# Optimization experiments

Hardware: AMD Instinct MI355X
Metric: run time of the kernel (lower is better)

Reference implementation:

```python
import jax, jax.numpy as jnp
import numpy as np

N, E, H, L = 20000, 640000, 128, 3
IN_NODE, IN_EDGE = 128, 128


def _ln(x):
    m = jnp.mean(x, -1, keepdims=True)
    v = jnp.mean((x - m) ** 2, -1, keepdims=True)
    return (x - m) / jnp.sqrt(v + 1e-5)


def _multi_aggr(msg, dst, n):
    # PyG MultiAggregation(['mean','std','max','min']) -> concat on feature dim
    cnt = jax.ops.segment_sum(jnp.ones((msg.shape[0],), msg.dtype), dst, n)
    denom = jnp.maximum(cnt, 1.0)[:, None]
    mean = jax.ops.segment_sum(msg, dst, n) / denom
    mean2 = jax.ops.segment_sum(msg * msg, dst, n) / denom
    std = jnp.sqrt(jax.nn.relu(mean2 - mean * mean) + 1e-5)  # PyG StdAggregation
    has = (cnt > 0)[:, None]
    mx = jnp.where(has, jax.ops.segment_max(msg, dst, n), 0.0)
    mn = jnp.where(has, jax.ops.segment_min(msg, dst, n), 0.0)
    return jnp.concatenate([mean, std, mx, mn], axis=-1)  # [n, 4H]


def _pna(h, src, dst, ea, W1, b1, W2, b2, W3, b3, W4, b4, Wd, bd, n):
    # flow='source_to_target': j = src = edge_index[0], i = dst = edge_index[1]
    x1 = jax.nn.silu(h @ W1 + b1)  # lin1 -> x_j
    z = jax.nn.silu(h @ W2 + b2)   # lin2 -> z_i
    msg = z[dst] * x1[src] * ea    # message = z_i * x_j * edge_attr
    ret_node = _multi_aggr(msg, dst, n) @ Wd + bd
    ret_edge = jax.nn.silu(h @ W3 + b3)[src] * jax.nn.silu(h @ W4 + b4)[dst] * ea
    return ret_node, ret_edge


def _gnn(x, edge_index, edge_attr, Wn, bn, We, be, W1, b1, W2, b2, W3, b3, W4, b4,
         Wd, bd, Wnd1, bnd1, Wnd2, bnd2, Wed1, bed1, Wed2, bed2):
    n = x.shape[0]
    h = Wn.shape[1]
    src, dst = edge_index[0], edge_index[1]
    inv = jnp.concatenate([jnp.ones((h // 2,), x.dtype), -jnp.ones(((h + 1) // 2,), x.dtype)])
    hidden = x @ Wn + bn
    in_ea = edge_attr
    ea = edge_attr @ We + be
    for i in range(W1.shape[0]):
        hn = _ln(hidden)
        rn1, re1 = _pna(hn, src, dst, ea, W1[i], b1[i], W2[i], b2[i], W3[i], b3[i], W4[i], b4[i], Wd[i], bd[i], n)
        rn2, re2 = _pna(hn, dst, src, inv * ea, W1[i], b1[i], W2[i], b2[i], W3[i], b3[i], W4[i], b4[i], Wd[i], bd[i], n)
        hidden = hidden + rn1 + rn2
        ea = ea + re1 + inv * re2
    node_pred = x + 0.01 * (jax.nn.silu(_ln(hidden) @ Wnd1 + bnd1) @ Wnd2 + bnd2)
    edge_pred = in_ea + 0.01 * (jax.nn.silu(_ln(ea) @ Wed1 + bed1) @ Wed2 + bed2)
    return node_pred, edge_pred


def setup_inputs() -> dict:
    key = jax.random.key(0)
    ks = jax.random.split(key, 20)
    g = lambda k, s, sc=0.05: jax.random.normal(k, s, jnp.float32) * sc
    return {
        "x": g(ks[0], (N, IN_NODE), 1.0),
        "edge_attr": g(ks[1], (E, IN_EDGE), 1.0),
        "Wn": g(ks[2], (IN_NODE, H)), "bn": jnp.zeros((H,), jnp.float32),
        "We": g(ks[3], (IN_EDGE, H)), "be": jnp.zeros((H,), jnp.float32),
        "W1": g(ks[4], (L, H, H)), "b1": jnp.zeros((L, H), jnp.float32),
        "W2": g(ks[5], (L, H, H)), "b2": jnp.zeros((L, H), jnp.float32),
        "W3": g(ks[6], (L, H, H)), "b3": jnp.zeros((L, H), jnp.float32),
        "W4": g(ks[7], (L, H, H)), "b4": jnp.zeros((L, H), jnp.float32),
        "Wd": g(ks[8], (L, 4 * H, H)), "bd": jnp.zeros((L, H), jnp.float32),
        "Wnd1": g(ks[9], (H, H)), "bnd1": jnp.zeros((H,), jnp.float32),
        "Wnd2": g(ks[10], (H, IN_NODE)), "bnd2": jnp.zeros((IN_NODE,), jnp.float32),
        "Wed1": g(ks[11], (H, H)), "bed1": jnp.zeros((H,), jnp.float32),
        "Wed2": g(ks[12], (H, IN_EDGE)), "bed2": jnp.zeros((IN_EDGE,), jnp.float32),
        "edge_index": jax.random.randint(ks[13], (2, E), 0, N),
    }


def reference(x, edge_attr, Wn, bn, We, be, W1, b1, W2, b2, W3, b3, W4, b4, Wd, bd,
              Wnd1, bnd1, Wnd2, bnd2, Wed1, bed1, Wed2, bed2, edge_index):
    return _gnn(x, edge_index, edge_attr, Wn, bn, We, be, W1, b1, W2, b2, W3, b3,
                W4, b4, Wd, bd, Wnd1, bnd1, Wnd2, bnd2, Wed1, bed1, Wed2, bed2)
```

## Files before the change

kernel.cpp:

```cpp
#include <hip/hip_runtime.h>
#include <cstdint>
#include <cstddef>

typedef __attribute__((ext_vector_type(8))) short short8x;
typedef __attribute__((ext_vector_type(4))) float f32x4;

static constexpr int NN = 20000;
static constexpr int EE = 640000;
static constexpr int NT_E = EE / 128;
static constexpr int NPAIR = NT_E / 2;

#define DEVI __device__ __forceinline__

DEVI float b2f(uint16_t u){ union{uint32_t i; float f;} x; x.i = (uint32_t)u<<16; return x.f; }
DEVI uint16_t f2b(float f){ union{float f; uint32_t i;} x; x.f=f; uint32_t i=x.i;
  return (uint16_t)((i + 0x7FFFu + ((i>>16)&1u))>>16); }
DEVI float silu_f(float v){ return v / (1.f + __expf(-v)); }

DEVI uint4 pack8(float4 a, float4 b){
  union{uint16_t u[8]; uint4 q;} pk;
  pk.u[0]=f2b(a.x); pk.u[1]=f2b(a.y); pk.u[2]=f2b(a.z); pk.u[3]=f2b(a.w);
  pk.u[4]=f2b(b.x); pk.u[5]=f2b(b.y); pk.u[6]=f2b(b.z); pk.u[7]=f2b(b.w);
  return pk.q;
}
DEVI uint2 pack4(float4 a){
  union{uint16_t u[4]; uint2 q;} pk;
  pk.u[0]=f2b(a.x); pk.u[1]=f2b(a.y); pk.u[2]=f2b(a.z); pk.u[3]=f2b(a.w);
  return pk.q;
}
DEVI float4 unpk4(uint2 v){
  return (float4){ b2f((uint16_t)(v.x & 0xFFFFu)), b2f((uint16_t)(v.x >> 16)),
                   b2f((uint16_t)(v.y & 0xFFFFu)), b2f((uint16_t)(v.y >> 16)) };
}

DEVI void ln8(float4& a, float4& b){
  float s = a.x+a.y+a.z+a.w + b.x+b.y+b.z+b.w;
  float q = a.x*a.x+a.y*a.y+a.z*a.z+a.w*a.w + b.x*b.x+b.y*b.y+b.z*b.z+b.w*b.w;
#pragma unroll
  for (int d=1; d<16; d<<=1){ s += __shfl_xor(s,d); q += __shfl_xor(q,d); }
  float m = s * 0.0078125f;
  float rstd = rsqrtf(fmaxf(q*0.0078125f - m*m, 0.f) + 1e-5f);
  a.x=(a.x-m)*rstd; a.y=(a.y-m)*rstd; a.z=(a.z-m)*rstd; a.w=(a.w-m)*rstd;
  b.x=(b.x-m)*rstd; b.y=(b.y-m)*rstd; b.z=(b.z-m)*rstd; b.w=(b.w-m)*rstd;
}

template<int AF32, int LNA, int EPI, int SILU>
__global__ __launch_bounds__(256) void gemm_node(
    const void* Ap, const uint16_t* __restrict__ Wt,
    const float* __restrict__ bias, float bias_scale,
    int M, int K,
    uint16_t* outb, float* outf,
    const float* __restrict__ resid, float resid_scale)
{
  __shared__ uint16_t Als[128*136];
  __shared__ uint16_t Wls[128*136];
  const int t = threadIdx.x;
  const int row0 = blockIdx.x * 128;
  const int w = t >> 6, l = t & 63;
  const int lr = l & 15, lk = (l>>4)*8;

  f32x4 acc[2][8];
#pragma unroll
  for (int a=0;a<2;a++)
#pragma unroll
    for(int b=0;b<8;b++) acc[a][b] = (f32x4){0.f,0.f,0.f,0.f};

  for (int kc = 0; kc < K; kc += 128){
#pragma unroll
    for (int i=0;i<8;i++){
      int c = t + i*256;
      int r = c >> 4, k8 = (c & 15)*8;
      int gr = row0 + r;
      if (AF32){
        float4 a = {0.f,0.f,0.f,0.f}, b = {0.f,0.f,0.f,0.f};
        if (gr < M){
          const float* Af = (const float*)Ap + (size_t)gr*K + kc + k8;
          a = *(const float4*)Af; b = *(const float4*)(Af + 4);
        }
        if (LNA) ln8(a, b);
        *(uint4*)(&Als[r*136 + k8]) = pack8(a, b);
      } else {
        uint4 v = {0u,0u,0u,0u};
        if (gr < M) v = *(const uint4*)((const uint16_t*)Ap + (size_t)gr*K + kc + k8);
        *(uint4*)(&Als[r*136 + k8]) = v;
      }
    }
#pragma unroll
    for (int i=0;i<8;i++){
      int c = t + i*256;
      int r = c >> 4, k8 = (c & 15)*8;
      *(uint4*)(&Wls[r*136 + k8]) = *(const uint4*)(Wt + (size_t)r*K + kc + k8);
    }
    __syncthreads();
#pragma unroll
    for (int kt=0; kt<4; ++kt){
      int kb = kt*32 + lk;
      short8x bfr[8];
#pragma unroll
      for (int c16=0;c16<8;c16++) bfr[c16] = *(const short8x*)(&Wls[(c16*16+lr)*136 + kb]);
#pragma unroll
      for (int r16=0;r16<2;r16++){
        short8x afr = *(const short8x*)(&Als[(w*32 + r16*16 + lr)*136 + kb]);
#pragma unroll
        for (int c16=0;c16<8;c16++)
          acc[r16][c16] = __builtin_amdgcn_mfma_f32_16x16x32_bf16(bfr[c16], afr, acc[r16][c16], 0,0,0);
      }
    }
    __syncthreads();
  }

  float4 bbv[8];
#pragma unroll
  for (int c16=0;c16<8;c16++){
    float4 b4 = *(const float4*)(bias + c16*16 + (l>>4)*4);
    bbv[c16] = (float4){b4.x*bias_scale, b4.y*bias_scale, b4.z*bias_scale, b4.w*bias_scale};
  }
#pragma unroll
  for (int r16=0;r16<2;r16++){
    int row = row0 + w*32 + r16*16 + lr;
    if (row >= M) continue;
#pragma unroll
    for (int c16=0;c16<8;c16++){
      int colb = c16*16 + (l>>4)*4;
      float4 v = (float4){acc[r16][c16][0]+bbv[c16].x, acc[r16][c16][1]+bbv[c16].y,
                          acc[r16][c16][2]+bbv[c16].z, acc[r16][c16][3]+bbv[c16].w};
      if (SILU){ v.x=silu_f(v.x); v.y=silu_f(v.y); v.z=silu_f(v.z); v.w=silu_f(v.w); }
      size_t o = (size_t)row*128 + colb;
      if (EPI==0)      *(uint2*)(outb + o) = pack4(v);
      else if (EPI==1) *(float4*)(outf + o) = v;
      else if (EPI==2){ float4 old = *(const float4*)(outf + o);
        *(float4*)(outf + o) = (float4){old.x+v.x, old.y+v.y, old.z+v.z, old.w+v.w}; }
      else { float4 r = *(const float4*)(resid + o);
        *(float4*)(outf + o) = (float4){r.x+resid_scale*v.x, r.y+resid_scale*v.y,
                                        r.z+resid_scale*v.z, r.w+resid_scale*v.w}; }
    }
  }
}

__global__ __launch_bounds__(256) void proj4(
    const float* __restrict__ hidden, const uint16_t* __restrict__ Wt4,
    const float* __restrict__ b0p, const float* __restrict__ b1p,
    const float* __restrict__ b2p, const float* __restrict__ b3p,
    uint16_t* o0, uint16_t* o1, uint16_t* o2, uint16_t* o3, int M)
{
  __shared__ uint16_t Als[128*136];
  __shared__ uint16_t Wls[2][128*136];
  const int t = threadIdx.x;
  const int row0 = blockIdx.x * 128;
  const int w = t >> 6, l = t & 63;
  const int lr = l & 15, lk = (l>>4)*8;

#pragma unroll
  for (int i=0;i<8;i++){
    int c = t + i*256;
    int r = c >> 4, k8 = (c & 15)*8;
    int gr = row0 + r;
    float4 a = {0.f,0.f,0.f,0.f}, b = {0.f,0.f,0.f,0.f};
    if (gr < M){
      const float* Af = hidden + (size_t)gr*128 + k8;
      a = *(const float4*)Af; b = *(const float4*)(Af + 4);
    }
    ln8(a, b);
    *(uint4*)(&Als[r*136 + k8]) = pack8(a, b);
  }
#pragma unroll
  for (int i=0;i<8;i++){
    int c = t + i*256;
    int r = c >> 4, k8 = (c & 15)*8;
    *(uint4*)(&Wls[0][r*136 + k8]) = *(const uint4*)(Wt4 + (size_t)r*128 + k8);
  }
  __syncthreads();

#pragma unroll
  for (int p=0; p<4; ++p){
    if (p < 3){
#pragma unroll
      for (int i=0;i<8;i++){
        int c = t + i*256;
        int r = c >> 4, k8 = (c & 15)*8;
        *(uint4*)(&Wls[(p+1)&1][r*136 + k8]) =
          *(const uint4*)(Wt4 + (size_t)(p+1)*16384 + (size_t)r*128 + k8);
      }
    }
    f32x4 acc[2][8];
#pragma unroll
    for (int a=0;a<2;a++)
#pragma unroll
      for(int b=0;b<8;b++) acc[a][b] = (f32x4){0.f,0.f,0.f,0.f};
#pragma unroll
    for (int kt=0; kt<4; ++kt){
      int kb = kt*32 + lk;
      short8x bfr[8];
#pragma unroll
      for (int c16=0;c16<8;c16++) bfr[c16] = *(const short8x*)(&Wls[p&1][(c16*16+lr)*136 + kb]);
#pragma unroll
      for (int r16=0;r16<2;r16++){
        short8x afr = *(const short8x*)(&Als[(w*32 + r16*16 + lr)*136 + kb]);
#pragma unroll
        for (int c16=0;c16<8;c16++)
          acc[r16][c16] = __builtin_amdgcn_mfma_f32_16x16x32_bf16(bfr[c16], afr, acc[r16][c16], 0,0,0);
      }
    }
    const float* bp = (p==0)?b0p:(p==1)?b1p:(p==2)?b2p:b3p;
    uint16_t* op = (p==0)?o0:(p==1)?o1:(p==2)?o2:o3;
#pragma unroll
    for (int r16=0;r16<2;r16++){
      int row = row0 + w*32 + r16*16 + lr;
      if (row >= M) continue;
#pragma unroll
      for (int c16=0;c16<8;c16++){
        int colb = c16*16 + (l>>4)*4;
        float4 b4 = *(const float4*)(bp + colb);
        float4 v = (float4){silu_f(acc[r16][c16][0]+b4.x), silu_f(acc[r16][c16][1]+b4.y),
                            silu_f(acc[r16][c16][2]+b4.z), silu_f(acc[r16][c16][3]+b4.w)};
        *(uint2*)(op + (size_t)row*128 + colb) = pack4(v);
      }
    }
    __syncthreads();
  }
}

__global__ __launch_bounds__(256, 2) void enc_edge(
    const float* __restrict__ A, const uint16_t* __restrict__ Wt,
    const float* __restrict__ bias, float* __restrict__ outf)
{
  __shared__ uint16_t Als[128*136];
  __shared__ uint16_t Wls[128*136];
  const int t = threadIdx.x;
  const int w = t >> 6, l = t & 63;
  const int lr = l & 15, lk = (l>>4)*8;

#pragma unroll
  for (int i=0;i<8;i++){
    int c = t + i*256;
    int r = c >> 4, k8 = (c & 15)*8;
    *(uint4*)(&Wls[r*136 + k8]) = *(const uint4*)(Wt + (size_t)r*128 + k8);
  }
  float4 bbv[8];
#pragma unroll
  for (int c16=0;c16<8;c16++) bbv[c16] = *(const float4*)(bias + c16*16 + (l>>4)*4);

  int tile = blockIdx.x;
  float4 va[16];
#pragma unroll
  for (int i=0;i<8;i++){
    int c = t + i*256; int r = c>>4, k8 = (c&15)*8;
    const float* Af = A + ((size_t)tile*128 + r)*128 + k8;
    va[2*i] = *(const float4*)Af; va[2*i+1] = *(const float4*)(Af + 4);
  }
  while (tile < NT_E){
#pragma unroll
    for (int i=0;i<8;i++){
      int c = t + i*256; int r = c>>4, k8 = (c&15)*8;
      *(uint4*)(&Als[r*136 + k8]) = pack8(va[2*i], va[2*i+1]);
    }
    int next = tile + (int)gridDim.x;
    if (next < NT_E){
#pragma unroll
      for (int i=0;i<8;i++){
        int c = t + i*256; int r = c>>4, k8 = (c&15)*8;
        const float* Af = A + ((size_t)next*128 + r)*128 + k8;
        va[2*i] = *(const float4*)Af; va[2*i+1] = *(const float4*)(Af + 4);
      }
    }
    __syncthreads();
    f32x4 acc[2][8];
#pragma unroll
    for (int a=0;a<2;a++)
#pragma unroll
      for(int b=0;b<8;b++) acc[a][b] = (f32x4){0.f,0.f,0.f,0.f};
#pragma unroll
    for (int kt=0; kt<4; ++kt){
      int kb = kt*32 + lk;
      short8x bfr[8];
#pragma unroll
      for (int c16=0;c16<8;c16++) bfr[c16] = *(const short8x*)(&Wls[(c16*16+lr)*136 + kb]);
#pragma unroll
      for (int r16=0;r16<2;r16++){
        short8x afr = *(const short8x*)(&Als[(w*32 + r16*16 + lr)*136 + kb]);
#pragma unroll
        for (int c16=0;c16<8;c16++)
          acc[r16][c16] = __builtin_amdgcn_mfma_f32_16x16x32_bf16(bfr[c16], afr, acc[r16][c16], 0,0,0);
      }
    }
#pragma unroll
    for (int r16=0;r16<2;r16++){
      size_t row = (size_t)tile*128 + w*32 + r16*16 + lr;
#pragma unroll
      for (int c16=0;c16<8;c16++){
        int colb = c16*16 + (l>>4)*4;
        *(float4*)(outf + row*128 + colb) =
          (float4){acc[r16][c16][0]+bbv[c16].x, acc[r16][c16][1]+bbv[c16].y,
                   acc[r16][c16][2]+bbv[c16].z, acc[r16][c16][3]+bbv[c16].w};
      }
    }
    __syncthreads();
    tile = next;
  }
}

__global__ __launch_bounds__(512) void dec_edge(
    const float* __restrict__ ea, const float* __restrict__ eatt,
    const uint16_t* __restrict__ W1t, const uint16_t* __restrict__ W2t,
    const float* __restrict__ b1, const float* __restrict__ b2,
    float* __restrict__ outf)
{
  __shared__ uint16_t Als[2][128*136];
  __shared__ uint16_t W1ls[128*136];
  __shared__ uint16_t W2ls[128*136];
  const int t = threadIdx.x;
  const int half = t >> 8, th = t & 255;
  const int w = t >> 6, l = t & 63;
  const int lr = l & 15, lk = (l>>4)*8;
  const int tsel = w >> 2, wloc = w & 3;

#pragma unroll
  for (int i=0;i<4;i++){
    int c = t + i*512;
    int r = c >> 4, k8 = (c & 15)*8;
    *(uint4*)(&W1ls[r*136 + k8]) = *(const uint4*)(W1t + (size_t)r*128 + k8);
    *(uint4*)(&W2ls[r*136 + k8]) = *(const uint4*)(W2t + (size_t)r*128 + k8);
  }
  float bb1[8];
  float4 bb2v[8];
#pragma unroll
  for (int c16=0;c16<8;c16++){
    bb1[c16] = b1[c16*16+lr];
    bb2v[c16] = *(const float4*)(b2 + c16*16 + (l>>4)*4);
  }

  int pr = blockIdx.x;
  float4 va[16];
  float4 vet[16];
#pragma unroll
  for (int i=0;i<8;i++){
    int c = th + i*256; int r = c>>4, k8 = (c&15)*8;
    const float* Af = ea + ((size_t)pr*256 + half*128 + r)*128 + k8;
    va[2*i] = *(const float4*)Af; va[2*i+1] = *(const float4*)(Af + 4);
  }
#pragma unroll
  for (int r16=0;r16<2;r16++)
#pragma unroll
    for (int c16=0;c16<8;c16++){
      size_t row = (size_t)pr*256 + tsel*128 + wloc*32 + r16*16 + lr;
      vet[r16*8+c16] = *(const float4*)(eatt + row*128 + c16*16 + (l>>4)*4);
    }

  while (pr < NPAIR){
#pragma unroll
    for (int i=0;i<8;i++){
      int c = th + i*256; int r = c>>4, k8 = (c&15)*8;
      float4 a = va[2*i], b = va[2*i+1];
      ln8(a, b);
      *(uint4*)(&Als[half][r*136 + k8]) = pack8(a, b);
    }
    int nx = pr + (int)gridDim.x;
    if (nx < NPAIR){
#pragma unroll
      for (int i=0;i<8;i++){
        int c = th + i*256; int r = c>>4, k8 = (c&15)*8;
        const float* Af = ea + ((size_t)nx*256 + half*128 + r)*128 + k8;
        va[2*i] = *(const float4*)Af; va[2*i+1] = *(const float4*)(Af + 4);
      }
    }
    __syncthreads();

    f32x4 acc[2][8];
#pragma unroll
    for (int a=0;a<2;a++)
#pragma unroll
      for(int b=0;b<8;b++) acc[a][b] = (f32x4){0.f,0.f,0.f,0.f};
#pragma unroll
    for (int kt=0; kt<4; ++kt){
      int kb = kt*32 + lk;
      short8x bfr[8];
#pragma unroll
      for (int c16=0;c16<8;c16++) bfr[c16] = *(const short8x*)(&W1ls[(c16*16+lr)*136 + kb]);
#pragma unroll
      for (int r16=0;r16<2;r16++){
        short8x afr = *(const short8x*)(&Als[tsel][(wloc*32 + r16*16 + lr)*136 + kb]);
#pragma unroll
        for (int c16=0;c16<8;c16++)
          acc[r16][c16] = __builtin_amdgcn_mfma_f32_16x16x32_bf16(afr, bfr[c16], acc[r16][c16], 0,0,0);
      }
    }
#pragma unroll
    for (int r16=0;r16<2;r16++)
#pragma unroll
      for (int c16=0;c16<8;c16++)
#pragma unroll
        for (int j=0;j<4;j++){
          int rloc = wloc*32 + r16*16 + (l>>4)*4 + j;
          Als[tsel][rloc*136 + c16*16 + lr] = f2b(silu_f(acc[r16][c16][j] + bb1[c16]));
        }
    f32x4 acc2[2][8];
#pragma unroll
    for (int a=0;a<2;a++)
#pragma unroll
      for(int b=0;b<8;b++) acc2[a][b] = (f32x4){0.f,0.f,0.f,0.f};
#pragma unroll
    for (int kt=0; kt<4; ++kt){
      int kb = kt*32 + lk;
      short8x bfr[8];
#pragma unroll
      for (int c16=0;c16<8;c16++) bfr[c16] = *(const short8x*)(&W2ls[(c16*16+lr)*136 + kb]);
#pragma unroll
      for (int r16=0;r16<2;r16++){
        short8x afr = *(const short8x*)(&Als[tsel][(wloc*32 + r16*16 + lr)*136 + kb]);
#pragma unroll
        for (int c16=0;c16<8;c16++)
          acc2[r16][c16] = __builtin_amdgcn_mfma_f32_16x16x32_bf16(bfr[c16], afr, acc2[r16][c16], 0,0,0);
      }
    }
#pragma unroll
    for (int r16=0;r16<2;r16++){
      size_t row = (size_t)pr*256 + tsel*128 + wloc*32 + r16*16 + lr;
#pragma unroll
      for (int c16=0;c16<8;c16++){
        int colb = c16*16 + (l>>4)*4;
        float4 e = vet[r16*8+c16];
        *(float4*)(outf + row*128 + colb) =
          (float4){e.x + 0.01f*(acc2[r16][c16][0]+bb2v[c16].x),
                   e.y + 0.01f*(acc2[r16][c16][1]+bb2v[c16].y),
                   e.z + 0.01f*(acc2[r16][c16][2]+bb2v[c16].z),
                   e.w + 0.01f*(acc2[r16][c16][3]+bb2v[c16].w)};
      }
    }
    if (nx < NPAIR){
#pragma unroll
      for (int r16=0;r16<2;r16++)
#pragma unroll
        for (int c16=0;c16<8;c16++){
          size_t row = (size_t)nx*256 + tsel*128 + wloc*32 + r16*16 + lr;
          vet[r16*8+c16] = *(const float4*)(eatt + row*128 + c16*16 + (l>>4)*4);
        }
    }
    __syncthreads();
    pr = nx;
  }
}

template<int INV, int EUPD, int ACCUM>
__global__ __launch_bounds__(128) void agg_kernel(
    const float* __restrict__ ea, float* ea_out,
    const uint16_t* __restrict__ x1, const uint16_t* __restrict__ z,
    const uint16_t* __restrict__ h3, const uint16_t* __restrict__ h4,
    const int* __restrict__ eids, const int* __restrict__ ptr,
    const int* __restrict__ other, uint16_t* stats)
{
  __shared__ int se[128];
  __shared__ int so[128];
  __shared__ float red[4][4][128];
  const int i = blockIdx.x, t = threadIdx.x;
  const int g = t >> 5, q = t & 31;
  const int f0 = q*4;
  float4 zi = unpk4(*(const uint2*)(z + (size_t)i*128 + f0));
  float4 h3i = {0,0,0,0}, h4i = {0,0,0,0};
  if (EUPD){
    h3i = unpk4(*(const uint2*)(h3 + (size_t)i*128 + f0));
    h4i = unpk4(*(const uint2*)(h4 + (size_t)i*128 + f0));
  }
  const int beg = ptr[i], end = ptr[i+1];
  float4 s={0,0,0,0}, s2={0,0,0,0};
  float4 mx={-3.4e38f,-3.4e38f,-3.4e38f,-3.4e38f}, mn={3.4e38f,3.4e38f,3.4e38f,3.4e38f};
  for (int jb = beg; jb < end; jb += 128){
    int cn = min(128, end - jb);
    if (t < cn){ int e = eids[jb+t]; se[t] = e; so[t] = other[e]; }
    __syncthreads();
#pragma unroll 2
    for (int jj = g; jj < cn; jj += 4){
      int e = se[jj], o = so[jj];
      float4 xo = unpk4(*(const uint2*)(x1 + (size_t)o*128 + f0));
      float4 ev = *(const float4*)(ea + (size_t)e*128 + f0);
      float4 m = (float4){zi.x*xo.x*ev.x, zi.y*xo.y*ev.y, zi.z*xo.z*ev.z, zi.w*xo.w*ev.w};
      if (INV){ if (q >= 16){ m.x=-m.x; m.y=-m.y; m.z=-m.z; m.w=-m.w; } }
      s.x+=m.x; s.y+=m.y; s.z+=m.z; s.w+=m.w;
      s2.x+=m.x*m.x; s2.y+=m.y*m.y; s2.z+=m.z*m.z; s2.w+=m.w*m.w;
      mx.x=fmaxf(mx.x,m.x); mx.y=fmaxf(mx.y,m.y); mx.z=fmaxf(mx.z,m.z); mx.w=fmaxf(mx.w,m.w);
      mn.x=fminf(mn.x,m.x); mn.y=fminf(mn.y,m.y); mn.z=fminf(mn.z,m.z); mn.w=fminf(mn.w,m.w);
      if (EUPD){
        float4 h3o = unpk4(*(const uint2*)(h3 + (size_t)o*128 + f0));
        float4 h4o = unpk4(*(const uint2*)(h4 + (size_t)o*128 + f0));
        *(float4*)(ea_out + (size_t)e*128 + f0) =
          (float4){ev.x*(1.f + h3o.x*h4i.x + h3i.x*h4o.x),
                   ev.y*(1.f + h3o.y*h4i.y + h3i.y*h4o.y),
                   ev.z*(1.f + h3o.z*h4i.z + h3i.z*h4o.z),
                   ev.w*(1.f + h3o.w*h4i.w + h3i.w*h4o.w)};
      }
    }
    __syncthreads();
  }
  *(float4*)(&red[g][0][f0]) = s;
  *(float4*)(&red[g][1][f0]) = s2;
  *(float4*)(&red[g][2][f0]) = mx;
  *(float4*)(&red[g][3][f0]) = mn;
  __syncthreads();
  float fs = red[0][0][t]+red[1][0][t]+red[2][0][t]+red[3][0][t];
  float fq = red[0][1][t]+red[1][1][t]+red[2][1][t]+red[3][1][t];
  float fmx = fmaxf(fmaxf(red[0][2][t],red[1][2][t]), fmaxf(red[2][2][t],red[3][2][t]));
  float fmn = fminf(fminf(red[0][3][t],red[1][3][t]), fminf(red[2][3][t],red[3][3][t]));
  int cnt = end - beg;
  float dn = cnt > 0 ? 1.f/(float)cnt : 1.f;
  float mean = fs*dn, m2 = fq*dn;
  float sd = sqrtf(fmaxf(m2 - mean*mean, 0.f) + 1e-5f);
  if (cnt == 0){ fmx = 0.f; fmn = 0.f; }
  size_t o0 = (size_t)i*512 + t;
  if (ACCUM){
    stats[o0    ] = f2b(b2f(stats[o0    ]) + mean);
    stats[o0+128] = f2b(b2f(stats[o0+128]) + sd);
    stats[o0+256] = f2b(b2f(stats[o0+256]) + fmx);
    stats[o0+384] = f2b(b2f(stats[o0+384]) + fmn);
  } else {
    stats[o0]=f2b(mean); stats[o0+128]=f2b(sd); stats[o0+256]=f2b(fmx); stats[o0+384]=f2b(fmn);
  }
}

__global__ void count_deg(const int* __restrict__ ei, int* cnt_src, int* cnt_dst){
  int e = blockIdx.x*256 + threadIdx.x;
  if (e < EE){
    atomicAdd(&cnt_src[ei[e]], 1);
    atomicAdd(&cnt_dst[ei[EE+e]], 1);
  }
}

__global__ __launch_bounds__(1024) void scan20k(const int* __restrict__ cnt, int* ptr){
  __shared__ int buf[1024];
  constexpr int C = 20;
  int t = threadIdx.x;
  int base = t*C;
  int loc[C];
  int sum = 0;
#pragma unroll
  for (int j=0;j<C;j++){
    int idx = base+j;
    int v = (idx < NN) ? cnt[idx] : 0;
    loc[j] = sum; sum += v;
  }
  buf[t] = sum;
  __syncthreads();
  for (int sft=1; sft<1024; sft<<=1){
    int add = (t>=sft) ? buf[t-sft] : 0;
    __syncthreads();
    buf[t] += add;
    __syncthreads();
  }
  int excl = buf[t] - sum;
#pragma unroll
  for (int j=0;j<C;j++){
    int idx = base+j;
    if (idx < NN) ptr[idx] = excl + loc[j];
  }
  if (t == 1023) ptr[NN] = buf[1023];
}

__global__ void init_cursor(const int* p1, int* c1, const int* p2, int* c2, int n){
  int i = blockIdx.x*256 + threadIdx.x;
  if (i < n){ c1[i] = p1[i]; c2[i] = p2[i]; }
}

__global__ void scatter_edges(const int* __restrict__ ei, int* cur_src, int* cur_dst,
                              int* eid_src, int* eid_dst){
  int e = blockIdx.x*256 + threadIdx.x;
  if (e < EE){
    int s = ei[e], d = ei[EE+e];
    eid_src[atomicAdd(&cur_src[s],1)] = e;
    eid_dst[atomicAdd(&cur_dst[d],1)] = e;
  }
}

__global__ void transpose_w(const float* __restrict__ W, uint16_t* __restrict__ Wt,
                            int K, int total){
  int idx = blockIdx.x*256 + threadIdx.x;
  if (idx < total){
    int per = K*128;
    int m = idx / per, r = idx - m*per;
    int k = r >> 7, c = r & 127;
    Wt[(size_t)m*per + (size_t)c*K + k] = f2b(W[idx]);
  }
}

extern "C" void kernel_launch(void* const* d_in, const int* in_sizes, int n_in,
                              void* d_out, int out_size, void* d_ws, size_t ws_size,
                              hipStream_t stream)
{
  const float* x    = (const float*)d_in[0];
  const float* eatt = (const float*)d_in[1];
  const float* Wn   = (const float*)d_in[2];
  const float* bn   = (const float*)d_in[3];
  const float* We   = (const float*)d_in[4];
  const float* be   = (const float*)d_in[5];
  const float* W1   = (const float*)d_in[6];
  const float* b1   = (const float*)d_in[7];
  const float* W2   = (const float*)d_in[8];
  const float* b2   = (const float*)d_in[9];
  const float* W3   = (const float*)d_in[10];
  const float* b3   = (const float*)d_in[11];
  const float* W4   = (const float*)d_in[12];
  const float* b4   = (const float*)d_in[13];
  const float* Wd   = (const float*)d_in[14];
  const float* bd   = (const float*)d_in[15];
  const float* Wnd1 = (const float*)d_in[16];
  const float* bnd1 = (const float*)d_in[17];
  const float* Wnd2 = (const float*)d_in[18];
  const float* bnd2 = (const float*)d_in[19];
  const float* Wed1 = (const float*)d_in[20];
  const float* bed1 = (const float*)d_in[21];
  const float* Wed2 = (const float*)d_in[22];
  const float* bed2 = (const float*)d_in[23];
  const int* ei     = (const int*)d_in[24];

  float* out_node = (float*)d_out;
  float* out_edge = out_node + (size_t)NN*128;
  float* ea = out_edge;

  char* p = (char*)d_ws;
  auto alloc = [&](size_t bytes)->char*{
    char* r = p; p += (bytes + 255) & ~(size_t)255; return r; };

  float*    hidden = (float*)   alloc((size_t)NN*128*4);
  uint16_t* x1b    = (uint16_t*)alloc((size_t)NN*128*2);
  uint16_t* zb     = (uint16_t*)alloc((size_t)NN*128*2);
  uint16_t* h3b    = (uint16_t*)alloc((size_t)NN*128*2);
  uint16_t* h4b    = (uint16_t*)alloc((size_t)NN*128*2);
  uint16_t* stats  = (uint16_t*)alloc((size_t)NN*512*2);
  int* cnt_src = (int*)alloc((size_t)NN*4);
  int* cnt_dst = (int*)alloc((size_t)NN*4);
  int* ptr_src = (int*)alloc((size_t)(NN+1)*4);
  int* ptr_dst = (int*)alloc((size_t)(NN+1)*4);
  int* cur_src = (int*)alloc((size_t)NN*4);
  int* cur_dst = (int*)alloc((size_t)NN*4);
  int* eid_src = (int*)alloc((size_t)EE*4);
  int* eid_dst = (int*)alloc((size_t)EE*4);
  uint16_t* WT = (uint16_t*)alloc((size_t)491520*2);

  uint16_t* wnT   = WT;
  uint16_t* weT   = WT + 16384;
  uint16_t* w1T   = WT + 32768;
  uint16_t* w2T   = WT + 81920;
  uint16_t* w3T   = WT + 131072;
  uint16_t* w4T   = WT + 180224;
  uint16_t* wdT   = WT + 229376;
  uint16_t* wnd1T = WT + 425984;
  uint16_t* wnd2T = WT + 442368;
  uint16_t* wed1T = WT + 458752;
  uint16_t* wed2T = WT + 475136;

  uint16_t* wp4 = (uint16_t*)alloc((size_t)3*4*16384*2);

  hipMemsetAsync(cnt_src, 0, (size_t)NN*4, stream);
  hipMemsetAsync(cnt_dst, 0, (size_t)NN*4, stream);
  count_deg<<<(EE+255)/256, 256, 0, stream>>>(ei, cnt_src, cnt_dst);
  scan20k<<<1, 1024, 0, stream>>>(cnt_src, ptr_src);
  scan20k<<<1, 1024, 0, stream>>>(cnt_dst, ptr_dst);
  init_cursor<<<(NN+255)/256, 256, 0, stream>>>(ptr_src, cur_src, ptr_dst, cur_dst, NN);
  scatter_edges<<<(EE+255)/256, 256, 0, stream>>>(ei, cur_src, cur_dst, eid_src, eid_dst);

  transpose_w<<<64, 256, 0, stream>>>(Wn, wnT, 128, 16384);
  transpose_w<<<64, 256, 0, stream>>>(We, weT, 128, 16384);
  transpose_w<<<192, 256, 0, stream>>>(W1, w1T, 128, 49152);
  transpose_w<<<192, 256, 0, stream>>>(W2, w2T, 128, 49152);
  transpose_w<<<192, 256, 0, stream>>>(W3, w3T, 128, 49152);
  transpose_w<<<192, 256, 0, stream>>>(W4, w4T, 128, 49152);
  transpose_w<<<768, 256, 0, stream>>>(Wd, wdT, 512, 196608);
  transpose_w<<<64, 256, 0, stream>>>(Wnd1, wnd1T, 128, 16384);
  transpose_w<<<64, 256, 0, stream>>>(Wnd2, wnd2T, 128, 16384);
  transpose_w<<<64, 256, 0, stream>>>(Wed1, wed1T, 128, 16384);
  transpose_w<<<64, 256, 0, stream>>>(Wed2, wed2T, 128, 16384);
  for (int lyr = 0; lyr < 3; ++lyr){
    hipMemcpyAsync(wp4 + (size_t)lyr*65536 +     0, w1T + lyr*16384, 32768, hipMemcpyDeviceToDevice, stream);
    hipMemcpyAsync(wp4 + (size_t)lyr*65536 + 16384, w2T + lyr*16384, 32768, hipMemcpyDeviceToDevice, stream);
    hipMemcpyAsync(wp4 + (size_t)lyr*65536 + 32768, w3T + lyr*16384, 32768, hipMemcpyDeviceToDevice, stream);
    hipMemcpyAsync(wp4 + (size_t)lyr*65536 + 49152, w4T + lyr*16384, 32768, hipMemcpyDeviceToDevice, stream);
  }

  const int gN = (NN+127)/128;

  gemm_node<1,0,1,0><<<gN, 256, 0, stream>>>(x, wnT, bn, 1.f, NN, 128, nullptr, hidden, nullptr, 0.f);
  enc_edge<<<512, 256, 0, stream>>>(eatt, weT, be, ea);

  for (int lyr = 0; lyr < 3; ++lyr){
    const uint16_t* wdl = wdT + lyr*65536;
    proj4<<<gN, 256, 0, stream>>>(hidden, wp4 + (size_t)lyr*65536,
                                  b1 + lyr*128, b2 + lyr*128, b3 + lyr*128, b4 + lyr*128,
                                  x1b, zb, h3b, h4b, NN);
    agg_kernel<1,0,0><<<NN, 128, 0, stream>>>(ea, nullptr, x1b, zb, nullptr, nullptr,
                                              eid_src, ptr_src, ei + EE, stats);
    agg_kernel<0,1,1><<<NN, 128, 0, stream>>>(ea, ea, x1b, zb, h3b, h4b,
                                              eid_dst, ptr_dst, ei, stats);
    gemm_node<0,0,2,0><<<gN, 256, 0, stream>>>(stats, wdl, bd + lyr*128, 2.f, NN, 512, nullptr, hidden, nullptr, 0.f);
  }

  gemm_node<1,1,0,1><<<gN, 256, 0, stream>>>(hidden, wnd1T, bnd1, 1.f, NN, 128, x1b, nullptr, nullptr, 0.f);
  gemm_node<0,0,3,0><<<gN, 256, 0, stream>>>(x1b, wnd2T, bnd2, 1.f, NN, 128, nullptr, out_node, x, 0.01f);

  dec_edge<<<256, 512, 0, stream>>>(ea, eatt, wed1T, wed2T, bed1, bed2, out_edge);
}
```

Baseline: 1.705 ms.

## Store edge features in bf16 workspace and simplify edge encoder/decoder kernels

Keeps the running edge-feature tensor in a bf16 workspace buffer when there is room, instead of fp32 in the output buffer. This halves the bytes moved by the edge-bound aggregation kernels in every layer. The edge encoder and decoder are rewritten to read MFMA fragments straight from global memory, one tile per block, with no persistent loop and no shared-memory staging. W1-W4 are now transposed straight into the packed layout, removing the device copies. The cost is extra rounding error that builds up in edge features over the three layers.

After: 1.401 ms. -17.8%, faster.

```diff
diff --git a/kernel.cpp b/kernel.cpp
--- a/kernel.cpp
+++ b/kernel.cpp
@@ -8,7 +8,6 @@
 static constexpr int NN = 20000;
 static constexpr int EE = 640000;
 static constexpr int NT_E = EE / 128;
-static constexpr int NPAIR = NT_E / 2;
 
 #define DEVI __device__ __forceinline__
 
@@ -31,6 +30,36 @@
 DEVI float4 unpk4(uint2 v){
   return (float4){ b2f((uint16_t)(v.x & 0xFFFFu)), b2f((uint16_t)(v.x >> 16)),
                    b2f((uint16_t)(v.y & 0xFFFFu)), b2f((uint16_t)(v.y >> 16)) };
+}
+DEVI short8x pk_frag(float4 a, float4 b){
+  union{uint16_t u[8]; short8x s;} pk;
+  pk.u[0]=f2b(a.x); pk.u[1]=f2b(a.y); pk.u[2]=f2b(a.z); pk.u[3]=f2b(a.w);
+  pk.u[4]=f2b(b.x); pk.u[5]=f2b(b.y); pk.u[6]=f2b(b.z); pk.u[7]=f2b(b.w);
+  return pk.s;
+}
+
+template<typename EAT>
+DEVI void load8e(const EAT* base, size_t row, int col8, float4& a, float4& b){
+  if constexpr (sizeof(EAT)==2){
+    uint4 v = *(const uint4*)((const uint16_t*)base + row*128 + col8);
+    a = (float4){b2f((uint16_t)(v.x&0xFFFFu)), b2f((uint16_t)(v.x>>16)),
+                 b2f((uint16_t)(v.y&0xFFFFu)), b2f((uint16_t)(v.y>>16))};
+    b = (float4){b2f((uint16_t)(v.z&0xFFFFu)), b2f((uint16_t)(v.z>>16)),
+                 b2f((uint16_t)(v.w&0xFFFFu)), b2f((uint16_t)(v.w>>16))};
+  } else {
+    const float* f = (const float*)base + row*128 + col8;
+    a = *(const float4*)f; b = *(const float4*)(f+4);
+  }
+}
+template<typename EAT>
+DEVI void store4e(EAT* base, size_t idx, float4 v){
+  if constexpr (sizeof(EAT)==2) *(uint2*)((uint16_t*)base + idx) = pack4(v);
+  else *(float4*)((float*)base + idx) = v;
+}
+template<typename EAT>
+DEVI float4 ld4e(const EAT* base, size_t idx){
+  if constexpr (sizeof(EAT)==2) return unpk4(*(const uint2*)((const uint16_t*)base + idx));
+  else return *(const float4*)((const float*)base + idx);
 }
 
 DEVI void ln8(float4& a, float4& b){
@@ -220,229 +249,151 @@
   }
 }
 
+template<typename EAT>
 __global__ __launch_bounds__(256, 2) void enc_edge(
     const float* __restrict__ A, const uint16_t* __restrict__ Wt,
-    const float* __restrict__ bias, float* __restrict__ outf)
+    const float* __restrict__ bias, EAT* __restrict__ out)
 {
-  __shared__ uint16_t Als[128*136];
-  __shared__ uint16_t Wls[128*136];
-  const int t = threadIdx.x;
-  const int w = t >> 6, l = t & 63;
-  const int lr = l & 15, lk = (l>>4)*8;
-
-#pragma unroll
-  for (int i=0;i<8;i++){
-    int c = t + i*256;
-    int r = c >> 4, k8 = (c & 15)*8;
-    *(uint4*)(&Wls[r*136 + k8]) = *(const uint4*)(Wt + (size_t)r*128 + k8);
-  }
-  float4 bbv[8];
-#pragma unroll
-  for (int c16=0;c16<8;c16++) bbv[c16] = *(const float4*)(bias + c16*16 + (l>>4)*4);
-
-  int tile = blockIdx.x;
-  float4 va[16];
-#pragma unroll
-  for (int i=0;i<8;i++){
-    int c = t + i*256; int r = c>>4, k8 = (c&15)*8;
-    const float* Af = A + ((size_t)tile*128 + r)*128 + k8;
-    va[2*i] = *(const float4*)Af; va[2*i+1] = *(const float4*)(Af + 4);
-  }
-  while (tile < NT_E){
-#pragma unroll
-    for (int i=0;i<8;i++){
-      int c = t + i*256; int r = c>>4, k8 = (c&15)*8;
-      *(uint4*)(&Als[r*136 + k8]) = pack8(va[2*i], va[2*i+1]);
-    }
-    int next = tile + (int)gridDim.x;
-    if (next < NT_E){
-#pragma unroll
-      for (int i=0;i<8;i++){
-        int c = t + i*256; int r = c>>4, k8 = (c&15)*8;
-        const float* Af = A + ((size_t)next*128 + r)*128 + k8;
-        va[2*i] = *(const float4*)Af; va[2*i+1] = *(const float4*)(Af + 4);
-      }
-    }
-    __syncthreads();
-    f32x4 acc[2][8];
-#pragma unroll
-    for (int a=0;a<2;a++)
-#pragma unroll
-      for(int b=0;b<8;b++) acc[a][b] = (f32x4){0.f,0.f,0.f,0.f};
-#pragma unroll
-    for (int kt=0; kt<4; ++kt){
-      int kb = kt*32 + lk;
-      short8x bfr[8];
-#pragma unroll
-      for (int c16=0;c16<8;c16++) bfr[c16] = *(const short8x*)(&Wls[(c16*16+lr)*136 + kb]);
-#pragma unroll
-      for (int r16=0;r16<2;r16++){
-        short8x afr = *(const short8x*)(&Als[(w*32 + r16*16 + lr)*136 + kb]);
-#pragma unroll
-        for (int c16=0;c16<8;c16++)
-          acc[r16][c16] = __builtin_amdgcn_mfma_f32_16x16x32_bf16(bfr[c16], afr, acc[r16][c16], 0,0,0);
-      }
-    }
-#pragma unroll
-    for (int r16=0;r16<2;r16++){
-      size_t row = (size_t)tile*128 + w*32 + r16*16 + lr;
-#pragma unroll
-      for (int c16=0;c16<8;c16++){
-        int colb = c16*16 + (l>>4)*4;
-        *(float4*)(outf + row*128 + colb) =
-          (float4){acc[r16][c16][0]+bbv[c16].x, acc[r16][c16][1]+bbv[c16].y,
-                   acc[r16][c16][2]+bbv[c16].z, acc[r16][c16][3]+bbv[c16].w};
-      }
-    }
-    __syncthreads();
-    tile = next;
-  }
-}
-
-__global__ __launch_bounds__(512) void dec_edge(
-    const float* __restrict__ ea, const float* __restrict__ eatt,
+  const int t = threadIdx.x, w = t >> 6, l = t & 63;
+  const int lr = l & 15, g = l >> 4;
+  const size_t base = (size_t)blockIdx.x*128 + w*32;
+
+  short8x fr[2][4];
+#pragma unroll
+  for (int r16=0;r16<2;r16++){
+#pragma unroll
+    for (int kt=0;kt<4;kt++){
+      const float* Af = A + (base + r16*16 + lr)*128 + kt*32 + g*8;
+      float4 a = *(const float4*)Af, b = *(const float4*)(Af + 4);
+      fr[r16][kt] = pk_frag(a, b);
+    }
+  }
+  f32x4 acc[2][8];
+#pragma unroll
+  for (int a=0;a<2;a++)
+#pragma unroll
+    for (int b=0;b<8;b++) acc[a][b] = (f32x4){0.f,0.f,0.f,0.f};
+#pragma unroll
+  for (int kt=0;kt<4;kt++){
+#pragma unroll
+    for (int c16=0;c16<8;c16++){
+      short8x bfr = *(const short8x*)(Wt + (size_t)(c16*16+lr)*128 + kt*32 + g*8);
+      acc[0][c16] = __builtin_amdgcn_mfma_f32_16x16x32_bf16(bfr, fr[0][kt], acc[0][c16], 0,0,0);
+      acc[1][c16] = __builtin_amdgcn_mfma_f32_16x16x32_bf16(bfr, fr[1][kt], acc[1][c16], 0,0,0);
+    }
+  }
+#pragma unroll
+  for (int r16=0;r16<2;r16++){
+    size_t row = base + r16*16 + lr;
+#pragma unroll
+    for (int c16=0;c16<8;c16++){
+      int colb = c16*16 + g*4;
+      float4 b4 = *(const float4*)(bias + colb);
+      store4e(out, row*128 + colb,
+        (float4){acc[r16][c16][0]+b4.x, acc[r16][c16][1]+b4.y,
+                 acc[r16][c16][2]+b4.z, acc[r16][c16][3]+b4.w});
+    }
+  }
+}
+
+template<typename EAT>
+__global__ __launch_bounds__(256, 2) void dec_edge(
+    const EAT* ea, const float* __restrict__ eatt,
     const uint16_t* __restrict__ W1t, const uint16_t* __restrict__ W2t,
     const float* __restrict__ b1, const float* __restrict__ b2,
-    float* __restrict__ outf)
+    float* outf)
 {
-  __shared__ uint16_t Als[2][128*136];
-  __shared__ uint16_t W1ls[128*136];
-  __shared__ uint16_t W2ls[128*136];
-  const int t = threadIdx.x;
-  const int half = t >> 8, th = t & 255;
-  const int w = t >> 6, l = t & 63;
-  const int lr = l & 15, lk = (l>>4)*8;
-  const int tsel = w >> 2, wloc = w & 3;
-
-#pragma unroll
-  for (int i=0;i<4;i++){
-    int c = t + i*512;
-    int r = c >> 4, k8 = (c & 15)*8;
-    *(uint4*)(&W1ls[r*136 + k8]) = *(const uint4*)(W1t + (size_t)r*128 + k8);
-    *(uint4*)(&W2ls[r*136 + k8]) = *(const uint4*)(W2t + (size_t)r*128 + k8);
-  }
-  float bb1[8];
-  float4 bb2v[8];
+  __shared__ uint16_t Pls[4][32*136];
+  const int t = threadIdx.x, w = t >> 6, l = t & 63;
+  const int lr = l & 15, g = l >> 4;
+  uint16_t* Ps = &Pls[w][0];
+  const size_t base = (size_t)blockIdx.x*128 + w*32;
+
+  short8x fr[2][4];
+#pragma unroll
+  for (int r16=0;r16<2;r16++){
+    float4 va[4][2];
+    float s=0.f, q=0.f;
+#pragma unroll
+    for (int kt=0;kt<4;kt++){
+      load8e(ea, base + r16*16 + lr, kt*32 + g*8, va[kt][0], va[kt][1]);
+      float4 a = va[kt][0], b = va[kt][1];
+      s += a.x+a.y+a.z+a.w + b.x+b.y+b.z+b.w;
+      q += a.x*a.x+a.y*a.y+a.z*a.z+a.w*a.w + b.x*b.x+b.y*b.y+b.z*b.z+b.w*b.w;
+    }
+    s += __shfl_xor(s,16); q += __shfl_xor(q,16);
+    s += __shfl_xor(s,32); q += __shfl_xor(q,32);
+    float m = s*0.0078125f;
+    float rstd = rsqrtf(fmaxf(q*0.0078125f - m*m, 0.f) + 1e-5f);
+#pragma unroll
+    for (int kt=0;kt<4;kt++){
+      float4 a = va[kt][0], b = va[kt][1];
+      a.x=(a.x-m)*rstd; a.y=(a.y-m)*rstd; a.z=(a.z-m)*rstd; a.w=(a.w-m)*rstd;
+      b.x=(b.x-m)*rstd; b.y=(b.y-m)*rstd; b.z=(b.z-m)*rstd; b.w=(b.w-m)*rstd;
+      fr[r16][kt] = pk_frag(a, b);
+    }
+  }
+  f32x4 acc[2][8];
+#pragma unroll
+  for (int a=0;a<2;a++)
+#pragma unroll
+    for (int b=0;b<8;b++) acc[a][b] = (f32x4){0.f,0.f,0.f,0.f};
+#pragma unroll
+  for (int kt=0;kt<4;kt++){
+#pragma unroll
+    for (int c16=0;c16<8;c16++){
+      short8x bfr = *(const short8x*)(W1t + (size_t)(c16*16+lr)*128 + kt*32 + g*8);
+      acc[0][c16] = __builtin_amdgcn_mfma_f32_16x16x32_bf16(fr[0][kt], bfr, acc[0][c16], 0,0,0);
+      acc[1][c16] = __builtin_amdgcn_mfma_f32_16x16x32_bf16(fr[1][kt], bfr, acc[1][c16], 0,0,0);
+    }
+  }
 #pragma unroll
   for (int c16=0;c16<8;c16++){
-    bb1[c16] = b1[c16*16+lr];
-    bb2v[c16] = *(const float4*)(b2 + c16*16 + (l>>4)*4);
-  }
-
-  int pr = blockIdx.x;
-  float4 va[16];
-  float4 vet[16];
-#pragma unroll
-  for (int i=0;i<8;i++){
-    int c = th + i*256; int r = c>>4, k8 = (c&15)*8;
-    const float* Af = ea + ((size_t)pr*256 + half*128 + r)*128 + k8;
-    va[2*i] = *(const float4*)Af; va[2*i+1] = *(const float4*)(Af + 4);
-  }
-#pragma unroll
-  for (int r16=0;r16<2;r16++)
+    float bb = b1[c16*16+lr];
+#pragma unroll
+    for (int r16=0;r16<2;r16++)
+#pragma unroll
+      for (int j=0;j<4;j++)
+        Ps[(r16*16 + g*4 + j)*136 + c16*16 + lr] = f2b(silu_f(acc[r16][c16][j] + bb));
+  }
+  f32x4 acc2[2][8];
+#pragma unroll
+  for (int a=0;a<2;a++)
+#pragma unroll
+    for (int b=0;b<8;b++) acc2[a][b] = (f32x4){0.f,0.f,0.f,0.f};
+#pragma unroll
+  for (int kt=0;kt<4;kt++){
+    short8x a0 = *(const short8x*)(Ps + (0*16 + lr)*136 + kt*32 + g*8);
+    short8x a1 = *(const short8x*)(Ps + (1*16 + lr)*136 + kt*32 + g*8);
 #pragma unroll
     for (int c16=0;c16<8;c16++){
-      size_t row = (size_t)pr*256 + tsel*128 + wloc*32 + r16*16 + lr;
-      vet[r16*8+c16] = *(const float4*)(eatt + row*128 + c16*16 + (l>>4)*4);
-    }
-
-  while (pr < NPAIR){
-#pragma unroll
-    for (int i=0;i<8;i++){
-      int c = th + i*256; int r = c>>4, k8 = (c&15)*8;
-      float4 a = va[2*i], b = va[2*i+1];
-      ln8(a, b);
-      *(uint4*)(&Als[half][r*136 + k8]) = pack8(a, b);
-    }
-    int nx = pr + (int)gridDim.x;
-    if (nx < NPAIR){
-#pragma unroll
-      for (int i=0;i<8;i++){
-        int c = th + i*256; int r = c>>4, k8 = (c&15)*8;
-        const float* Af = ea + ((size_t)nx*256 + half*128 + r)*128 + k8;
-        va[2*i] = *(const float4*)Af; va[2*i+1] = *(const float4*)(Af + 4);
-      }
-    }
-    __syncthreads();
-
-    f32x4 acc[2][8];
-#pragma unroll
-    for (int a=0;a<2;a++)
-#pragma unroll
-      for(int b=0;b<8;b++) acc[a][b] = (f32x4){0.f,0.f,0.f,0.f};
-#pragma unroll
-    for (int kt=0; kt<4; ++kt){
-      int kb = kt*32 + lk;
-      short8x bfr[8];
-#pragma unroll
-      for (int c16=0;c16<8;c16++) bfr[c16] = *(const short8x*)(&W1ls[(c16*16+lr)*136 + kb]);
-#pragma unroll
-      for (int r16=0;r16<2;r16++){
-        short8x afr = *(const short8x*)(&Als[tsel][(wloc*32 + r16*16 + lr)*136 + kb]);
-#pragma unroll
-        for (int c16=0;c16<8;c16++)
-          acc[r16][c16] = __builtin_amdgcn_mfma_f32_16x16x32_bf16(afr, bfr[c16], acc[r16][c16], 0,0,0);
-      }
-    }
-#pragma unroll
-    for (int r16=0;r16<2;r16++)
-#pragma unroll
-      for (int c16=0;c16<8;c16++)
-#pragma unroll
-        for (int j=0;j<4;j++){
-          int rloc = wloc*32 + r16*16 + (l>>4)*4 + j;
-          Als[tsel][rloc*136 + c16*16 + lr] = f2b(silu_f(acc[r16][c16][j] + bb1[c16]));
-        }
-    f32x4 acc2[2][8];
-#pragma unroll
-    for (int a=0;a<2;a++)
-#pragma unroll
-      for(int b=0;b<8;b++) acc2[a][b] = (f32x4){0.f,0.f,0.f,0.f};
-#pragma unroll
-    for (int kt=0; kt<4; ++kt){
-      int kb = kt*32 + lk;
-      short8x bfr[8];
-#pragma unroll
-      for (int c16=0;c16<8;c16++) bfr[c16] = *(const short8x*)(&W2ls[(c16*16+lr)*136 + kb]);
-#pragma unroll
-      for (int r16=0;r16<2;r16++){
-        short8x afr = *(const short8x*)(&Als[tsel][(wloc*32 + r16*16 + lr)*136 + kb]);
-#pragma unroll
-        for (int c16=0;c16<8;c16++)
-          acc2[r16][c16] = __builtin_amdgcn_mfma_f32_16x16x32_bf16(bfr[c16], afr, acc2[r16][c16], 0,0,0);
-      }
-    }
-#pragma unroll
-    for (int r16=0;r16<2;r16++){
-      size_t row = (size_t)pr*256 + tsel*128 + wloc*32 + r16*16 + lr;
-#pragma unroll
-      for (int c16=0;c16<8;c16++){
-        int colb = c16*16 + (l>>4)*4;
-        float4 e = vet[r16*8+c16];
-        *(float4*)(outf + row*128 + colb) =
-          (float4){e.x + 0.01f*(acc2[r16][c16][0]+bb2v[c16].x),
-                   e.y + 0.01f*(acc2[r16][c16][1]+bb2v[c16].y),
-                   e.z + 0.01f*(acc2[r16][c16][2]+bb2v[c16].z),
-                   e.w + 0.01f*(acc2[r16][c16][3]+bb2v[c16].w)};
-      }
-    }
-    if (nx < NPAIR){
-#pragma unroll
-      for (int r16=0;r16<2;r16++)
-#pragma unroll
-        for (int c16=0;c16<8;c16++){
-          size_t row = (size_t)nx*256 + tsel*128 + wloc*32 + r16*16 + lr;
-          vet[r16*8+c16] = *(const float4*)(eatt + row*128 + c16*16 + (l>>4)*4);
-        }
-    }
-    __syncthreads();
-    pr = nx;
-  }
-}
-
-template<int INV, int EUPD, int ACCUM>
+      short8x bfr = *(const short8x*)(W2t + (size_t)(c16*16+lr)*128 + kt*32 + g*8);
+      acc2[0][c16] = __builtin_amdgcn_mfma_f32_16x16x32_bf16(bfr, a0, acc2[0][c16], 0,0,0);
+      acc2[1][c16] = __builtin_amdgcn_mfma_f32_16x16x32_bf16(bfr, a1, acc2[1][c16], 0,0,0);
+    }
+  }
+#pragma unroll
+  for (int r16=0;r16<2;r16++){
+    size_t row = base + r16*16 + lr;
+    float4 et[8];
+#pragma unroll
+    for (int c16=0;c16<8;c16++) et[c16] = *(const float4*)(eatt + row*128 + c16*16 + g*4);
+#pragma unroll
+    for (int c16=0;c16<8;c16++){
+      int colb = c16*16 + g*4;
+      float4 bb = *(const float4*)(b2 + colb);
+      *(float4*)(outf + row*128 + colb) =
+        (float4){et[c16].x + 0.01f*(acc2[r16][c16][0]+bb.x),
+                 et[c16].y + 0.01f*(acc2[r16][c16][1]+bb.y),
+                 et[c16].z + 0.01f*(acc2[r16][c16][2]+bb.z),
+                 et[c16].w + 0.01f*(acc2[r16][c16][3]+bb.w)};
+    }
+  }
+}
+
+template<typename EAT, int INV, int EUPD, int ACCUM>
 __global__ __launch_bounds__(128) void agg_kernel(
-    const float* __restrict__ ea, float* ea_out,
+    const EAT* ea, EAT* ea_out,
     const uint16_t* __restrict__ x1, const uint16_t* __restrict__ z,
     const uint16_t* __restrict__ h3, const uint16_t* __restrict__ h4,
     const int* __restrict__ eids, const int* __restrict__ ptr,
@@ -471,7 +422,7 @@
     for (int jj = g; jj < cn; jj += 4){
       int e = se[jj], o = so[jj];
       float4 xo = unpk4(*(const uint2*)(x1 + (size_t)o*128 + f0));
-      float4 ev = *(const float4*)(ea + (size_t)e*128 + f0);
+      float4 ev = ld4e(ea, (size_t)e*128 + f0);
       float4 m = (float4){zi.x*xo.x*ev.x, zi.y*xo.y*ev.y, zi.z*xo.z*ev.z, zi.w*xo.w*ev.w};
       if (INV){ if (q >= 16){ m.x=-m.x; m.y=-m.y; m.z=-m.z; m.w=-m.w; } }
       s.x+=m.x; s.y+=m.y; s.z+=m.z; s.w+=m.w;
@@ -481,11 +432,11 @@
       if (EUPD){
         float4 h3o = unpk4(*(const uint2*)(h3 + (size_t)o*128 + f0));
         float4 h4o = unpk4(*(const uint2*)(h4 + (size_t)o*128 + f0));
-        *(float4*)(ea_out + (size_t)e*128 + f0) =
+        store4e(ea_out, (size_t)e*128 + f0,
           (float4){ev.x*(1.f + h3o.x*h4i.x + h3i.x*h4o.x),
                    ev.y*(1.f + h3o.y*h4i.y + h3i.y*h4o.y),
                    ev.z*(1.f + h3o.z*h4i.z + h3i.z*h4o.z),
-                   ev.w*(1.f + h3o.w*h4i.w + h3i.w*h4o.w)};
+                   ev.w*(1.f + h3o.w*h4i.w + h3i.w*h4o.w)});
       }
     }
     __syncthreads();
@@ -569,13 +520,13 @@
 }
 
 __global__ void transpose_w(const float* __restrict__ W, uint16_t* __restrict__ Wt,
-                            int K, int total){
+                            int K, int total, int ostride, int ooff){
   int idx = blockIdx.x*256 + threadIdx.x;
   if (idx < total){
     int per = K*128;
     int m = idx / per, r = idx - m*per;
     int k = r >> 7, c = r & 127;
-    Wt[(size_t)m*per + (size_t)c*K + k] = f2b(W[idx]);
+    Wt[(size_t)m*ostride + ooff + (size_t)c*K + k] = f2b(W[idx]);
   }
 }
 
@@ -611,7 +562,6 @@
 
   float* out_node = (float*)d_out;
   float* out_edge = out_node + (size_t)NN*128;
-  float* ea = out_edge;
 
   char* p = (char*)d_ws;
   auto alloc = [&](size_t bytes)->char*{
@@ -631,21 +581,22 @@
   int* cur_dst = (int*)alloc((size_t)NN*4);
   int* eid_src = (int*)alloc((size_t)EE*4);
   int* eid_dst = (int*)alloc((size_t)EE*4);
-  uint16_t* WT = (uint16_t*)alloc((size_t)491520*2);
+  uint16_t* WT  = (uint16_t*)alloc((size_t)294912*2);
+  uint16_t* wp4 = (uint16_t*)alloc((size_t)3*65536*2);
 
   uint16_t* wnT   = WT;
   uint16_t* weT   = WT + 16384;
-  uint16_t* w1T   = WT + 32768;
-  uint16_t* w2T   = WT + 81920;
-  uint16_t* w3T   = WT + 131072;
-  uint16_t* w4T   = WT + 180224;
-  uint16_t* wdT   = WT + 229376;
-  uint16_t* wnd1T = WT + 425984;
-  uint16_t* wnd2T = WT + 442368;
-  uint16_t* wed1T = WT + 458752;
-  uint16_t* wed2T = WT + 475136;
-
-  uint16_t* wp4 = (uint16_t*)alloc((size_t)3*4*16384*2);
+  uint16_t* wdT   = WT + 32768;
+  uint16_t* wnd1T = WT + 229376;
+  uint16_t* wnd2T = WT + 245760;
+  uint16_t* wed1T = WT + 262144;
+  uint16_t* wed2T = WT + 278528;
+
+  size_t used = (size_t)(p - (char*)d_ws);
+  bool ea16ok = (ws_size >= used + (size_t)EE*128*2 + 512);
+  uint16_t* ea16 = nullptr;
+  if (ea16ok) ea16 = (uint16_t*)alloc((size_t)EE*128*2);
+  float* eaf = out_edge;
 
   hipMemsetAsync(cnt_src, 0, (size_t)NN*4, stream);
   hipMemsetAsync(cnt_dst, 0, (size_t)NN*4, stream);
@@ -655,43 +606,55 @@
   init_cursor<<<(NN+255)/256, 256, 0, stream>>>(ptr_src, cur_src, ptr_dst, cur_dst, NN);
   scatter_edges<<<(EE+255)/256, 256, 0, stream>>>(ei, cur_src, cur_dst, eid_src, eid_dst);
 
-  transpose_w<<<64, 256, 0, stream>>>(Wn, wnT, 128, 16384);
-  transpose_w<<<64, 256, 0, stream>>>(We, weT, 128, 16384);
-  transpose_w<<<192, 256, 0, stream>>>(W1, w1T, 128, 49152);
-  transpose_w<<<192, 256, 0, stream>>>(W2, w2T, 128, 49152);
-  transpose_w<<<192, 256, 0, stream>>>(W3, w3T, 128, 49152);
-  transpose_w<<<192, 256, 0, stream>>>(W4, w4T, 128, 49152);
-  transpose_w<<<768, 256, 0, stream>>>(Wd, wdT, 512, 196608);
-  transpose_w<<<64, 256, 0, stream>>>(Wnd1, wnd1T, 128, 16384);
-  transpose_w<<<64, 256, 0, stream>>>(Wnd2, wnd2T, 128, 16384);
-  transpose_w<<<64, 256, 0, stream>>>(Wed1, wed1T, 128, 16384);
-  transpose_w<<<64, 256, 0, stream>>>(Wed2, wed2T, 128, 16384);
-  for (int lyr = 0; lyr < 3; ++lyr){
-    hipMemcpyAsync(wp4 + (size_t)lyr*65536 +     0, w1T + lyr*16384, 32768, hipMemcpyDeviceToDevice, stream);
-    hipMemcpyAsync(wp4 + (size_t)lyr*65536 + 16384, w2T + lyr*16384, 32768, hipMemcpyDeviceToDevice, stream);
-    hipMemcpyAsync(wp4 + (size_t)lyr*65536 + 32768, w3T + lyr*16384, 32768, hipMemcpyDeviceToDevice, stream);
-    hipMemcpyAsync(wp4 + (size_t)lyr*65536 + 49152, w4T + lyr*16384, 32768, hipMemcpyDeviceToDevice, stream);
-  }
+  transpose_w<<<64, 256, 0, stream>>>(Wn, wnT, 128, 16384, 16384, 0);
+  transpose_w<<<64, 256, 0, stream>>>(We, weT, 128, 16384, 16384, 0);
+  transpose_w<<<192, 256, 0, stream>>>(W1, wp4, 128, 49152, 65536, 0);
+  transpose_w<<<192, 256, 0, stream>>>(W2, wp4, 128, 49152, 65536, 16384);
+  transpose_w<<<192, 256, 0, stream>>>(W3, wp4, 128, 49152, 65536, 32768);
+  transpose_w<<<192, 256, 0, stream>>>(W4, wp4, 128, 49152, 65536, 49152);
+  transpose_w<<<768, 256, 0, stream>>>(Wd, wdT, 512, 196608, 65536, 0);
+  transpose_w<<<64, 256, 0, stream>>>(Wnd1, wnd1T, 128, 16384, 16384, 0);
+  transpose_w<<<64, 256, 0, stream>>>(Wnd2, wnd2T, 128, 16384, 16384, 0);
+  transpose_w<<<64, 256, 0, stream>>>(Wed1, wed1T, 128, 16384, 16384, 0);
+  transpose_w<<<64, 256, 0, stream>>>(Wed2, wed2T, 128, 16384, 16384, 0);
 
   const int gN = (NN+127)/128;
 
   gemm_node<1,0,1,0><<<gN, 256, 0, stream>>>(x, wnT, bn, 1.f, NN, 128, nullptr, hidden, nullptr, 0.f);
-  enc_edge<<<512, 256, 0, stream>>>(eatt, weT, be, ea);
-
-  for (int lyr = 0; lyr < 3; ++lyr){
-    const uint16_t* wdl = wdT + lyr*65536;
-    proj4<<<gN, 256, 0, stream>>>(hidden, wp4 + (size_t)lyr*65536,
-                                  b1 + lyr*128, b2 + lyr*128, b3 + lyr*128, b4 + lyr*128,
-                                  x1b, zb, h3b, h4b, NN);
-    agg_kernel<1,0,0><<<NN, 128, 0, stream>>>(ea, nullptr, x1b, zb, nullptr, nullptr,
-                                              eid_src, ptr_src, ei + EE, stats);
-    agg_kernel<0,1,1><<<NN, 128, 0, stream>>>(ea, ea, x1b, zb, h3b, h4b,
-                                              eid_dst, ptr_dst, ei, stats);
-    gemm_node<0,0,2,0><<<gN, 256, 0, stream>>>(stats, wdl, bd + lyr*128, 2.f, NN, 512, nullptr, hidden, nullptr, 0.f);
+
+  if (ea16ok){
+    enc_edge<uint16_t><<<NT_E, 256, 0, stream>>>(eatt, weT, be, ea16);
+    for (int lyr = 0; lyr < 3; ++lyr){
+      proj4<<<gN, 256, 0, stream>>>(hidden, wp4 + (size_t)lyr*65536,
+                                    b1 + lyr*128, b2 + lyr*128, b3 + lyr*128, b4 + lyr*128,
+                                    x1b, zb, h3b, h4b, NN);
+      agg_kernel<uint16_t,1,0,0><<<NN, 128, 0, stream>>>(ea16, nullptr, x1b, zb, nullptr, nullptr,
+                                                         eid_src, ptr_src, ei + EE, stats);
+      agg_kernel<uint16_t,0,1,1><<<NN, 128, 0, stream>>>(ea16, ea16, x1b, zb, h3b, h4b,
+                                                         eid_dst, ptr_dst, ei, stats);
+      gemm_node<0,0,2,0><<<gN, 256, 0, stream>>>(stats, wdT + lyr*65536, bd + lyr*128, 2.f,
+                                                 NN, 512, nullptr, hidden, nullptr, 0.f);
+    }
+  } else {
+    enc_edge<float><<<NT_E, 256, 0, stream>>>(eatt, weT, be, eaf);
+    for (int lyr = 0; lyr < 3; ++lyr){
+      proj4<<<gN, 256, 0, stream>>>(hidden, wp4 + (size_t)lyr*65536,
+                                    b1 + lyr*128, b2 + lyr*128, b3 + lyr*128, b4 + lyr*128,
+                                    x1b, zb, h3b, h4b, NN);
+      agg_kernel<float,1,0,0><<<NN, 128, 0, stream>>>(eaf, nullptr, x1b, zb, nullptr, nullptr,
+                                                      eid_src, ptr_src, ei + EE, stats);
+      agg_kernel<float,0,1,1><<<NN, 128, 0, stream>>>(eaf, eaf, x1b, zb, h3b, h4b,
+                                                      eid_dst, ptr_dst, ei, stats);
+      gemm_node<0,0,2,0><<<gN, 256, 0, stream>>>(stats, wdT + lyr*65536, bd + lyr*128, 2.f,
+                                                 NN, 512, nullptr, hidden, nullptr, 0.f);
+    }
   }
 
   gemm_node<1,1,0,1><<<gN, 256, 0, stream>>>(hidden, wnd1T, bnd1, 1.f, NN, 128, x1b, nullptr, nullptr, 0.f);
   gemm_node<0,0,3,0><<<gN, 256, 0, stream>>>(x1b, wnd2T, bnd2, 1.f, NN, 128, nullptr, out_node, x, 0.01f);
 
-  dec_edge<<<256, 512, 0, stream>>>(ea, eatt, wed1T, wed2T, bed1, bed2, out_edge);
-}
+  if (ea16ok)
+    dec_edge<uint16_t><<<NT_E, 256, 0, stream>>>(ea16, eatt, wed1T, wed2T, bed1, bed2, out_edge);
+  else
+    dec_edge<float><<<NT_E, 256, 0, stream>>>(eaf, eatt, wed1T, wed2T, bed1, bed2, out_edge);
+}
```
